# Kernel tuning notes

Hardware: AMD Instinct MI355X
Metric: run time of the kernel (lower is better)

## Reference

```python
import jax, jax.numpy as jnp
import numpy as np
from jax import lax

T, N, CIN, CMID, IMG, LABELS = 8, 32, 3, 64, 64, 10
W4 = IMG // 4  # 16 after two 2x2 maxpools
FC1_IN = CMID * W4 * W4                 # 16384
FC1_OUT = (CMID * W4 // 2) * W4 // 2    # 4096 (matches Python int-div precedence)
V_TH = 1.0
ALPHA = 4.0  # spikingjelly surrogate.Sigmoid default alpha

@jax.custom_vjp
def spike(x):
    # Heaviside(v - v_th); surrogate sigmoid gradient in bwd
    return (x >= 0.0).astype(x.dtype)

def _spike_fwd(x):
    return (x >= 0.0).astype(x.dtype), x

def _spike_bwd(x, g):
    s = jax.nn.sigmoid(ALPHA * x)
    return (g * ALPHA * s * (1.0 - s),)

spike.defvjp(_spike_fwd, _spike_bwd)

def if_node(x_seq):
    # IFNode, hard reset to v_reset=0, v starts at 0, multi-step over leading T axis
    def step(v, x):
        v = v + x                 # charge
        s = spike(v - V_TH)       # fire
        return v * (1.0 - s), s   # hard reset (reset path keeps grad: detach_reset=False)
    _, s_seq = lax.scan(step, jnp.zeros_like(x_seq[0]), x_seq)
    return s_seq

def conv2d(x, w):
    # kernel 3x3, stride 1, padding 1, no bias
    return lax.conv_general_dilated(x, w, (1, 1), ((1, 1), (1, 1)),
                                    dimension_numbers=('NCHW', 'OIHW', 'NCHW'))

def maxpool2(x):
    return lax.reduce_window(x, -jnp.inf, lax.max, (1, 1, 2, 2), (1, 1, 2, 2), 'VALID')

def seq_apply(f, x_seq):
    # stateless layer applied over merged [T*N, ...] (spikingjelly step_mode='m')
    t, n = x_seq.shape[:2]
    y = f(x_seq.reshape((t * n,) + x_seq.shape[2:]))
    return y.reshape((t, n) + y.shape[1:])


def setup_inputs() -> dict:
    key = jax.random.key(0)
    k = jax.random.split(key, 5)
    x_seq = jax.random.uniform(k[0], (T, N, CIN, IMG, IMG), dtype=jnp.float32)
    w1 = jax.random.normal(k[1], (CMID, CIN, 3, 3), dtype=jnp.float32) * (1.0 / np.sqrt(CIN * 9))
    w2 = jax.random.normal(k[2], (CMID, CMID, 3, 3), dtype=jnp.float32) * (1.0 / np.sqrt(CMID * 9))
    fc1 = jax.random.normal(k[3], (FC1_OUT, FC1_IN), dtype=jnp.float32) * (1.0 / np.sqrt(FC1_IN))
    fc2 = jax.random.normal(k[4], (LABELS, FC1_OUT), dtype=jnp.float32) * (1.0 / np.sqrt(FC1_OUT))
    return {"x_seq": x_seq, "w1": w1, "w2": w2, "fc1": fc1, "fc2": fc2}


def reference(x_seq, w1, w2, fc1, fc2):
    h = seq_apply(lambda x: conv2d(x, w1), x_seq)   # [T,N,64,64,64]
    h = if_node(h)
    h = seq_apply(maxpool2, h)                      # [T,N,64,32,32]
    h = seq_apply(lambda x: conv2d(x, w2), h)
    h = if_node(h)
    h = seq_apply(maxpool2, h)                      # [T,N,64,16,16]
    h = h.reshape(T, N, -1)                         # [T,N,16384]
    h = if_node(jnp.einsum('tni,oi->tno', h, fc1))  # [T,N,4096]
    h = if_node(jnp.einsum('tni,oi->tno', h, fc2))  # [T,N,10]
    return h.mean(axis=0)                           # firing rate over time: [N,10]
```

## Files before the change

### kernel.cpp

```cpp
#include <hip/hip_runtime.h>
#include <hip/hip_bf16.h>


#define T_STEPS 8
#define NB      32
#define CMID    64

typedef __bf16 bf16x2 __attribute__((ext_vector_type(2)));
typedef __bf16 bf16x4 __attribute__((ext_vector_type(4)));
typedef __bf16 bf16x8 __attribute__((ext_vector_type(8)));
typedef short  s16x8  __attribute__((ext_vector_type(8)));
typedef float  f32x4  __attribute__((ext_vector_type(4)));

struct Split3 { float h, m, l; };
__device__ __forceinline__ Split3 split3(float x) {
    Split3 s;
    __bf16 h = (__bf16)x;
    float r1 = x - (float)h;
    __bf16 m = (__bf16)r1;
    float r2 = r1 - (float)m;
    __bf16 l = (__bf16)r2;
    s.h = (float)h; s.m = (float)m; s.l = (float)l;
    return s;
}

__device__ __forceinline__ void split3v8(float4 a, float4 b,
                                         s16x8& fh, s16x8& fm, s16x8& fl) {
    float x[8] = {a.x, a.y, a.z, a.w, b.x, b.y, b.z, b.w};
    s16x8 h, m, l;
#pragma unroll
    for (int j = 0; j < 8; j++) {
        __bf16 ch = (__bf16)x[j];
        float r1 = x[j] - (float)ch;
        __bf16 cm = (__bf16)r1;
        float r2 = r1 - (float)cm;
        __bf16 cl = (__bf16)r2;
        h[j] = __builtin_bit_cast(short, ch);
        m[j] = __builtin_bit_cast(short, cm);
        l[j] = __builtin_bit_cast(short, cl);
    }
    fh = h; fm = m; fl = l;
}

__device__ __forceinline__ void load_lds16(const void* g, void* l) {
    __builtin_amdgcn_global_load_lds(
        (const __attribute__((address_space(1))) void*)g,
        (__attribute__((address_space(3))) void*)l, 16, 0, 0);
}

__global__ void k_w2s(const float* __restrict__ w2, __bf16* __restrict__ w2s) {
    int idx = blockIdx.x * 256 + threadIdx.x;
    int j    = idx & 7;
    int lane = (idx >> 3) & 63;
    int oh   = (idx >> 9) & 1;
    int kh   = (idx >> 10) & 1;
    int g    = idx >> 11;
    int tap  = g % 9;
    int ch   = g / 9;
    int co = ch * 32 + oh * 16 + (lane & 15);
    int ci = kh * 32 + (lane >> 4) * 8 + j;
    float w = w2[co * 576 + ci * 9 + tap];
    Split3 s = split3(w);
    __bf16* o = w2s + (((size_t)(g * 2 + kh) * 2 + oh) * 3) * 512 + lane * 8 + j;
    o[0]    = (__bf16)s.h;
    o[512]  = (__bf16)s.m;
    o[1024] = (__bf16)s.l;
}

__global__ __launch_bounds__(256) void k_conv1_if_pool(
        const float* __restrict__ x, const float* __restrict__ w1,
        __bf16* __restrict__ spk1p) {
    int b   = blockIdx.x;
    int n   = b >> 5;
    int cog = (b >> 2) & 7;
    int pht = b & 3;
    int tid = threadIdx.x;
    int pw  = tid & 31;
    int ph  = pht * 8 + (tid >> 5);
    int ih0 = 2 * ph - 1, iw0 = 2 * pw - 1;

    float v[8][4];
#pragma unroll
    for (int a = 0; a < 8; a++)
#pragma unroll
        for (int p = 0; p < 4; p++) v[a][p] = 0.f;

    for (int t = 0; t < T_STEPS; t++) {
        const float* xb = x + (size_t)(t * NB + n) * 3 * 4096;
        float patch[3][4][4];
#pragma unroll
        for (int ci = 0; ci < 3; ci++)
#pragma unroll
            for (int dy = 0; dy < 4; dy++) {
                int ih = ih0 + dy;
                bool rok = ((unsigned)ih < 64u);
#pragma unroll
                for (int dx = 0; dx < 4; dx++) {
                    int iw = iw0 + dx;
                    patch[ci][dy][dx] = (rok && ((unsigned)iw < 64u))
                                            ? xb[ci * 4096 + ih * 64 + iw] : 0.f;
                }
            }
        bf16x8 sv;
#pragma unroll
        for (int c8 = 0; c8 < 8; c8++) {
            int co = cog * 8 + c8;
            const float* wc = w1 + co * 27;
            float a0 = 0.f, a1 = 0.f, a2 = 0.f, a3 = 0.f;
#pragma unroll
            for (int ci = 0; ci < 3; ci++)
#pragma unroll
                for (int ky = 0; ky < 3; ky++)
#pragma unroll
                    for (int kx = 0; kx < 3; kx++) {
                        float w = wc[ci * 9 + ky * 3 + kx];
                        a0 += w * patch[ci][ky][kx];
                        a1 += w * patch[ci][ky][kx + 1];
                        a2 += w * patch[ci][ky + 1][kx];
                        a3 += w * patch[ci][ky + 1][kx + 1];
                    }
            float s0, s1, s2, s3;
            v[c8][0] += a0; s0 = (v[c8][0] >= 1.f) ? 1.f : 0.f; if (s0 > 0.f) v[c8][0] = 0.f;
            v[c8][1] += a1; s1 = (v[c8][1] >= 1.f) ? 1.f : 0.f; if (s1 > 0.f) v[c8][1] = 0.f;
            v[c8][2] += a2; s2 = (v[c8][2] >= 1.f) ? 1.f : 0.f; if (s2 > 0.f) v[c8][2] = 0.f;
            v[c8][3] += a3; s3 = (v[c8][3] >= 1.f) ? 1.f : 0.f; if (s3 > 0.f) v[c8][3] = 0.f;
            sv[c8] = (__bf16)fmaxf(fmaxf(s0, s1), fmaxf(s2, s3));
        }
        *(bf16x8*)(spk1p + ((size_t)(t * NB + n) * 1024 + ph * 32 + pw) * 64
                         + cog * 8) = sv;
    }
}

__global__ __launch_bounds__(512, 2) void k_conv2_if_pool(
        const short* __restrict__ spk1p,
        const short* __restrict__ w2s,
        __bf16* __restrict__ spk2) {
    int b     = blockIdx.x;
    int ch    = b & 1;
    int s2    = (b >> 1) & 3;
    int n     = b >> 3;
    int tid   = threadIdx.x;
    int lane  = tid & 63;
    int wv    = tid >> 6;
    int mh    = wv >> 1, oh = wv & 1;
    int lm    = lane & 15, kq = lane >> 4;

    __shared__ short Bs[55296];
    {
        const uint4* src = (const uint4*)(w2s + (size_t)ch * 55296);
        uint4* dst = (uint4*)Bs;
        for (int i = tid; i < 6912; i += 512) dst[i] = src[i];
    }
    __syncthreads();
    const short* Bsw = Bs + oh * 1536;

    f32x4 v[4];
#pragma unroll
    for (int i = 0; i < 4; i++) v[i] = (f32x4){0.f, 0.f, 0.f, 0.f};

    int co = ch * 32 + oh * 16 + lm;
    int pH = s2 * 4 + mh;
    int h0 = s2 * 8 + 2 * mh - 1;

#pragma unroll 1
    for (int t = 0; t < T_STEPS; t++) {
        const short* At = spk1p + (size_t)(t * NB + n) * 65536 + kq * 8;
        f32x4 acc[4];
#pragma unroll
        for (int i = 0; i < 4; i++) acc[i] = (f32x4){0.f, 0.f, 0.f, 0.f};

#pragma unroll 1
        for (int dy = 0; dy < 3; dy++) {
#pragma unroll 1
            for (int dx = 0; dx < 3; dx++) {
                const short* bp = Bsw + (dy * 3 + dx) * 6144 + lane * 8;
                s16x8 bf[2][3];
#pragma unroll
                for (int kh = 0; kh < 2; kh++)
#pragma unroll
                    for (int sp = 0; sp < 3; sp++)
                        bf[kh][sp] = *(const s16x8*)(bp + kh * 3072 + sp * 512);
#pragma unroll
                for (int i = 0; i < 4; i++) {
                    int hh = h0 + (i >> 1) + dy;
                    int ww = (i & 1) * 16 + lm + dx - 1;
                    bool ok = ((unsigned)hh < 32u) && ((unsigned)ww < 32u);
                    s16x8 a0 = {0, 0, 0, 0, 0, 0, 0, 0};
                    s16x8 a1 = {0, 0, 0, 0, 0, 0, 0, 0};
                    if (ok) {
                        const short* ap = At + (hh * 32 + ww) * 64;
                        a0 = *(const s16x8*)ap;
                        a1 = *(const s16x8*)(ap + 32);
                    }
#pragma unroll
                    for (int sp = 0; sp < 3; sp++) {
                        acc[i] = __builtin_amdgcn_mfma_f32_16x16x32_bf16(
                            a0, bf[0][sp], acc[i], 0, 0, 0);
                        acc[i] = __builtin_amdgcn_mfma_f32_16x16x32_bf16(
                            a1, bf[1][sp], acc[i], 0, 0, 0);
                    }
                }
            }
        }
        float s[4][4];
#pragma unroll
        for (int i = 0; i < 4; i++)
#pragma unroll
            for (int r = 0; r < 4; r++) {
                float vv = v[i][r] + acc[i][r];
                float sp = (vv >= 1.f) ? 1.f : 0.f;
                s[i][r] = sp;
                v[i][r] = (sp > 0.f) ? 0.f : vv;
            }
        __bf16* op = spk2 + ((size_t)(t * NB + n) * 64 + co) * 256 + pH * 16
                   + kq * 2;
#pragma unroll
        for (int i2 = 0; i2 < 2; i2++) {
            float p0 = fmaxf(fmaxf(s[i2][0], s[i2][1]),
                             fmaxf(s[i2 + 2][0], s[i2 + 2][1]));
            float p1 = fmaxf(fmaxf(s[i2][2], s[i2][3]),
                             fmaxf(s[i2 + 2][2], s[i2 + 2][3]));
            bf16x2 pv = {(__bf16)p0, (__bf16)p1};
            *(bf16x2*)(op + i2 * 8) = pv;
        }
    }
}

__global__ __launch_bounds__(512, 4) void k_fc1_mfma(
        const short* __restrict__ A,
        const float* __restrict__ W,
        float* __restrict__ part) {
    int b  = blockIdx.x;
    int nt = b & 63;
    int ks = b >> 6;
    int o0 = nt * 64;
    int kbase = ks * 2048;

    int tid  = threadIdx.x;
    int lane = tid & 63;
    int wv   = tid >> 6;
    int mq   = wv >> 1;
    int oh   = wv & 1;
    int lm   = lane & 15;
    int kq   = lane >> 4;

    __shared__ short Asm[2][8192];
    __shared__ float Wsm[2][2048];

    int wrow = tid >> 3;
    int wu   = (tid & 7) ^ (wrow & 7);
    const float* gW = W + (size_t)(o0 + wrow) * 16384 + kbase + wu * 4;
    const short* gA[2];
#pragma unroll
    for (int q = 0; q < 2; q++) {
        int p = q * 512 + tid;
        int r = p >> 2;
        int c = (p & 3) ^ ((r >> 1) & 3);
        gA[q] = A + (size_t)r * 16384 + kbase + c * 8;
    }

    int aoff[4];
#pragma unroll
    for (int i = 0; i < 4; i++) {
        int r = mq * 64 + i * 16 + lm;
        aoff[i] = (r * 4 + (kq ^ ((r >> 1) & 3))) * 8;
    }
    int woff[2][2];
#pragma unroll
    for (int oi = 0; oi < 2; oi++) {
        int row = (2 * oh + oi) * 16 + lm;
#pragma unroll
        for (int h = 0; h < 2; h++) {
            int u = kq * 2 + h;
            woff[oi][h] = (row * 8 + (u ^ (row & 7))) * 4;
        }
    }

    f32x4 acc[4][2];
#pragma unroll
    for (int i = 0; i < 4; i++)
#pragma unroll
        for (int oi = 0; oi < 2; oi++) acc[i][oi] = (f32x4){0.f, 0.f, 0.f, 0.f};

    load_lds16(gW, &Wsm[0][wv * 256]);
    load_lds16(gA[0], &Asm[0][wv * 512]);
    load_lds16(gA[1], &Asm[0][4096 + wv * 512]);
    __syncthreads();

#pragma unroll 1
    for (int it = 0; it < 64; ++it) {
        int bf = it & 1;
        if (it < 63) {
            load_lds16(gW + (it + 1) * 32, &Wsm[bf ^ 1][wv * 256]);
            load_lds16(gA[0] + (it + 1) * 32, &Asm[bf ^ 1][wv * 512]);
            load_lds16(gA[1] + (it + 1) * 32, &Asm[bf ^ 1][4096 + wv * 512]);
        }

        const short* as = Asm[bf];
        const float* ws = Wsm[bf];

        s16x8 av[4];
#pragma unroll
        for (int i = 0; i < 4; i++)
            av[i] = *(const s16x8*)(as + aoff[i]);

        float4 wraw[2][2];
#pragma unroll
        for (int oi = 0; oi < 2; oi++)
#pragma unroll
            for (int h = 0; h < 2; h++)
                wraw[oi][h] = *(const float4*)(ws + woff[oi][h]);

        s16x8 bfr[3][2];
#pragma unroll
        for (int oi = 0; oi < 2; oi++)
            split3v8(wraw[oi][0], wraw[oi][1],
                     bfr[0][oi], bfr[1][oi], bfr[2][oi]);

#pragma unroll
        for (int i = 0; i < 4; i++)
#pragma unroll
            for (int oi = 0; oi < 2; oi++) {
                acc[i][oi] = __builtin_amdgcn_mfma_f32_16x16x32_bf16(
                    av[i], bfr[0][oi], acc[i][oi], 0, 0, 0);
                acc[i][oi] = __builtin_amdgcn_mfma_f32_16x16x32_bf16(
                    av[i], bfr[1][oi], acc[i][oi], 0, 0, 0);
                acc[i][oi] = __builtin_amdgcn_mfma_f32_16x16x32_bf16(
                    av[i], bfr[2][oi], acc[i][oi], 0, 0, 0);
            }

        __syncthreads();
    }

    int col = lane & 15;
    int rq  = (lane >> 4) * 4;
#pragma unroll
    for (int i = 0; i < 4; i++)
#pragma unroll
        for (int oi = 0; oi < 2; oi++)
#pragma unroll
            for (int r = 0; r < 4; r++) {
                int m = mq * 64 + i * 16 + rq + r;
                int o = o0 + (2 * oh + oi) * 16 + col;
                part[((size_t)ks * 256 + m) * 4096 + o] = acc[i][oi][r];
            }
}

__global__ void k_fc1_if(const float* __restrict__ part,
                         float* __restrict__ spk3) {
    int idx = blockIdx.x * 256 + threadIdx.x;
    int o = idx & 4095;
    int n = idx >> 12;
    float v = 0.f;
    for (int t = 0; t < T_STEPS; t++) {
        int m = t * NB + n;
        float s = 0.f;
#pragma unroll
        for (int ks = 0; ks < 8; ks++)
            s += part[((size_t)ks * 256 + m) * 4096 + o];
        v += s;
        float sp = (v >= 1.f) ? 1.f : 0.f;
        if (sp > 0.f) v = 0.f;
        spk3[(size_t)m * 4096 + o] = sp;
    }
}

__global__ __launch_bounds__(256) void k_fc2_if_mean(
        const float* __restrict__ spk3, const float* __restrict__ fc2,
        float* __restrict__ out) {
    int b = blockIdx.x;
    int n = b / 10, o = b % 10;
    const float* wr = fc2 + o * 4096;
    __shared__ float red[256];
    int tid = threadIdx.x;
    float v = 0.f, cnt = 0.f;
    for (int t = 0; t < T_STEPS; t++) {
        const float* row = spk3 + (size_t)(t * NB + n) * 4096;
        float p = 0.f;
        for (int i = tid; i < 4096; i += 256) p += row[i] * wr[i];
        red[tid] = p;
        __syncthreads();
        for (int s = 128; s > 0; s >>= 1) {
            if (tid < s) red[tid] += red[tid + s];
            __syncthreads();
        }
        if (tid == 0) {
            v += red[0];
            float sp = (v >= 1.f) ? 1.f : 0.f;
            cnt += sp;
            if (sp > 0.f) v = 0.f;
        }
        __syncthreads();
    }
    if (tid == 0) out[n * 10 + o] = cnt * 0.125f;
}

extern "C" void kernel_launch(void* const* d_in, const int* in_sizes, int n_in,
                              void* d_out, int out_size, void* d_ws, size_t ws_size,
                              hipStream_t stream) {
    const float* x   = (const float*)d_in[0];
    const float* w1  = (const float*)d_in[1];
    const float* w2  = (const float*)d_in[2];
    const float* fc1 = (const float*)d_in[3];
    const float* fc2 = (const float*)d_in[4];
    float* out = (float*)d_out;

    float* ws = (float*)d_ws;
    const size_t off_w2s   = 0;
    const size_t off_spk1p = 57344;
    const size_t off_spk2  = off_spk1p + 8388608;
    const size_t off_part  = off_spk2 + 2097152;
    const size_t off_spk3  = off_part + 8388608;
    __bf16* w2s   = (__bf16*)(ws + off_w2s);
    __bf16* spk1p = (__bf16*)(ws + off_spk1p);
    __bf16* spk2  = (__bf16*)(ws + off_spk2);
    float*  part  = ws + off_part;
    float*  spk3  = ws + off_spk3;

    k_w2s<<<144, 256, 0, stream>>>(w2, w2s);
    k_conv1_if_pool<<<1024, 256, 0, stream>>>(x, w1, spk1p);
    k_conv2_if_pool<<<256, 512, 0, stream>>>((const short*)spk1p,
                                             (const short*)w2s, spk2);
    k_fc1_mfma<<<512, 512, 0, stream>>>((const short*)spk2, fc1, part);
    k_fc1_if<<<512, 256, 0, stream>>>(part, spk3);
    k_fc2_if_mean<<<320, 256, 0, stream>>>(spk3, fc2, out);
}
```

Before: 707.3 us.

## Stage conv2 input halo tile in LDS with swizzled layout per timestep

Conv2 now loads each timestep's input rows (with a one-pixel halo) into a zero-padded, XOR-swizzled shared-memory tile using async global-to-LDS copies. The 3x3 taps then read operands from LDS instead of doing repeated bounds-checked global loads. This removes redundant global traffic and the per-tap branching, at the cost of about 43 KB of extra LDS, which may reduce occupancy below two blocks per CU, plus extra barriers each timestep.

```diff
diff --git a/kernel.cpp b/kernel.cpp
--- a/kernel.cpp
+++ b/kernel.cpp
@@ -146,25 +146,50 @@
     int lm    = lane & 15, kq = lane >> 4;
 
     __shared__ short Bs[55296];
+    __shared__ short As[10 * 34 * 64];
+
     {
         const uint4* src = (const uint4*)(w2s + (size_t)ch * 55296);
         uint4* dst = (uint4*)Bs;
         for (int i = tid; i < 6912; i += 512) dst[i] = src[i];
+        uint4* za = (uint4*)As;
+        for (int i = tid; i < 2720; i += 512) za[i] = (uint4){0, 0, 0, 0};
     }
     __syncthreads();
     const short* Bsw = Bs + oh * 1536;
 
+    int wl  = lane >> 3;
+    int sph = lane & 7;
+
     f32x4 v[4];
 #pragma unroll
     for (int i = 0; i < 4; i++) v[i] = (f32x4){0.f, 0.f, 0.f, 0.f};
 
     int co = ch * 32 + oh * 16 + lm;
     int pH = s2 * 4 + mh;
-    int h0 = s2 * 8 + 2 * mh - 1;
 
 #pragma unroll 1
     for (int t = 0; t < T_STEPS; t++) {
-        const short* At = spk1p + (size_t)(t * NB + n) * 65536 + kq * 8;
+        const short* img = spk1p + (size_t)(t * NB + n) * 65536;
+
+        if (t > 0) __syncthreads();
+#pragma unroll
+        for (int q = 0; q < 5; q++) {
+            int u = q * 8 + wv;
+            int r = u >> 2;
+            int quarter = u & 3;
+            int hh = s2 * 8 - 1 + r;
+            if ((unsigned)hh < 32u) {
+                int widx = quarter * 8 + 1 + wl;
+                int slog = sph ^ (widx & 7);
+                const short* src = img + (size_t)(hh * 32 + widx - 1) * 64
+                                       + slog * 8;
+                short* dst = As + (r * 34 + quarter * 8 + 1) * 64;
+                load_lds16(src, dst);
+            }
+        }
+        __syncthreads();
+
         f32x4 acc[4];
 #pragma unroll
         for (int i = 0; i < 4; i++) acc[i] = (f32x4){0.f, 0.f, 0.f, 0.f};
@@ -182,16 +207,11 @@
                         bf[kh][sp] = *(const s16x8*)(bp + kh * 3072 + sp * 512);
 #pragma unroll
                 for (int i = 0; i < 4; i++) {
-                    int hh = h0 + (i >> 1) + dy;
-                    int ww = (i & 1) * 16 + lm + dx - 1;
-                    bool ok = ((unsigned)hh < 32u) && ((unsigned)ww < 32u);
-                    s16x8 a0 = {0, 0, 0, 0, 0, 0, 0, 0};
-                    s16x8 a1 = {0, 0, 0, 0, 0, 0, 0, 0};
-                    if (ok) {
-                        const short* ap = At + (hh * 32 + ww) * 64;
-                        a0 = *(const s16x8*)ap;
-                        a1 = *(const s16x8*)(ap + 32);
-                    }
+                    int r    = 2 * mh + (i >> 1) + dy;
+                    int widx = (i & 1) * 16 + lm + dx;
+                    const short* ap = As + (r * 34 + widx) * 64;
+                    s16x8 a0 = *(const s16x8*)(ap + ((kq    ) ^ (widx & 7)) * 8);
+                    s16x8 a1 = *(const s16x8*)(ap + ((kq + 4) ^ (widx & 7)) * 8);
 #pragma unroll
                     for (int sp = 0; sp < 3; sp++) {
                         acc[i] = __builtin_amdgcn_mfma_f32_16x16x32_bf16(
```

After: 632.4 us. 1.12x faster.
